# Performance work log

Measured on AMD Instinct MI355X. Metric: run time of the kernel, lower is better.

Reference implementation:

```python
import jax, jax.numpy as jnp
import numpy as np

N_SIGMA = 1
K_MAX = 8          # max number of non-zero instance ids
FG_W = 1.0         # foreground_weight
W_INST, W_VAR, W_SEED = 1.0, 10.0, 1.0


def _lovasz_hinge_flat(logits, labels_f):
    # logits, labels_f: [P] flat; standard Lovasz hinge (descending-error sort)
    signs = 2.0 * labels_f - 1.0
    errors = 1.0 - logits * signs
    perm = jnp.argsort(-errors)
    errors_sorted = errors[perm]
    gt_sorted = labels_f[perm]
    gts = gt_sorted.sum()
    cum = jnp.cumsum(gt_sorted)
    intersection = gts - cum
    union = gts + jnp.cumsum(1.0 - gt_sorted)
    jaccard = 1.0 - intersection / union
    grad = jnp.concatenate([jaccard[:1], jaccard[1:] - jaccard[:-1]])
    return jnp.sum(jax.nn.relu(errors_sorted) * jax.lax.stop_gradient(grad))


def _spatial_emb_loss(prediction, instances, labels):
    B, C, H, W = prediction.shape
    inst = instances[:, 0]  # [B,H,W]
    # coordinate buffer: linspace over the full 1024x2048 grid, then sliced
    xm = jnp.linspace(0.0, 2.0, 2048)[:W]
    ym = jnp.linspace(0.0, 1.0, 1024)[:H]
    xym = jnp.stack([jnp.broadcast_to(xm[None, :], (H, W)),
                     jnp.broadcast_to(ym[:, None], (H, W))])  # [2,H,W]
    ids = jnp.arange(1, K_MAX + 1)

    def per_image(pred, ins, lab):
        spatial_emb = jnp.tanh(pred[0:2]) + xym            # [2,H,W]
        sigma = pred[2]                                     # [H,W] (n_sigma=1)
        seed = jax.nn.sigmoid(pred[3])                      # [H,W]
        bg = (lab == 0)
        seed_loss_bg = jnp.sum(jnp.where(bg, seed ** 2, 0.0))
        masks = (ins[None] == ids[:, None, None])           # [K,H,W]
        mf = masks.astype(pred.dtype)
        counts = mf.sum((1, 2))                             # [K]
        present = counts > 0
        cnt = jnp.maximum(counts, 1.0)
        # to_center=True: center = mean of xym over instance pixels
        center = jnp.einsum('chw,khw->kc', xym, mf) / cnt[:, None]   # [K,2]
        s_mean = jnp.einsum('hw,khw->k', sigma, mf) / cnt            # [K]
        var_k = jnp.einsum('khw,khw->k',
                           (sigma[None] - jax.lax.stop_gradient(s_mean)[:, None, None]) ** 2,
                           mf) / cnt
        s_exp = jnp.exp(10.0 * s_mean)                                # [K]
        d2 = jnp.sum((spatial_emb[None] - center[:, :, None, None]) ** 2, axis=1)  # [K,H,W]
        dist = jnp.exp(-s_exp[:, None, None] * d2)                    # [K,H,W]
        lov = jax.vmap(_lovasz_hinge_flat)(2.0 * dist.reshape(K_MAX, -1) - 1.0,
                                           mf.reshape(K_MAX, -1))     # [K]
        seed_fg = jnp.einsum('khw,khw->k',
                             (seed[None] - jax.lax.stop_gradient(dist)) ** 2, mf)
        objf = jnp.maximum(present.sum().astype(pred.dtype), 1.0)
        inst_loss = jnp.where(present, lov, 0.0).sum() / objf
        var_loss = jnp.where(present, var_k, 0.0).sum() / objf
        seed_loss = (seed_loss_bg + FG_W * jnp.where(present, seed_fg, 0.0).sum()) / (H * W)
        return W_INST * inst_loss + W_VAR * var_loss + W_SEED * seed_loss

    per = jax.vmap(per_image)(prediction, inst, labels)
    return per.mean() + 0.0 * prediction.sum()


def setup_inputs() -> dict:
    key = jax.random.key(0)
    k1, k2, k3 = jax.random.split(key, 3)
    B, H, W = 4, 512, 1024
    prediction = jax.random.normal(k1, (B, 2 + N_SIGMA + 1, H, W), dtype=jnp.float32)
    instances = jax.random.randint(k2, (B, 1, H, W), 0, K_MAX + 1, dtype=jnp.int32)
    labels = jax.random.randint(k3, (B, H, W), 0, 2, dtype=jnp.int32)
    return {"prediction": prediction, "instances": instances, "labels": labels}


def reference(prediction, instances, labels):
    return _spatial_emb_loss(prediction, instances, labels)
```

## Files before the change

### kernel.cpp

```cpp
#include <hip/hip_runtime.h>
#include <math.h>

namespace {
constexpr int B_ = 4, K_ = 8, H_ = 512, W_ = 1024;
constexpr int N_ = H_ * W_;
constexpr int M_ = 256;
constexpr int MP_ = M_ + 1;
constexpr int BK_ = B_ * K_;
constexpr int KM_ = K_ * M_;

constexpr int HB_ = 2048;
constexpr int HBPB_ = HB_ / B_;
constexpr int HCH_ = N_ / HBPB_;
constexpr int SB_ = 1024;
constexpr int SBPB_ = SB_ / B_;
constexpr int SCH_ = N_ / SBPB_;
constexpr int NSTAT = 41;
constexpr int SLICES_ = 8;

constexpr size_t PART_BYTES  = (size_t)HB_ * KM_ * 4;
constexpr size_t SFG_OFF_B   = PART_BYTES;
constexpr size_t RED_OFF_B   = SFG_OFF_B + (size_t)BK_ * HBPB_ * 4;
constexpr size_t PSTAT_OFF_B = RED_OFF_B + (size_t)BK_ * SLICES_ * M_ * 8;
constexpr size_t WSF_OFF_B   = PSTAT_OFF_B + (size_t)B_ * NSTAT * SBPB_ * 4;

constexpr int CNT_OFF  = 0;
constexpr int BG_OFF   = 32;
constexpr int OBJF_OFF = 36;
constexpr int FIN_OFF  = 40;
}

__device__ __forceinline__ float fsigmoid_(float x) { return 1.0f / (1.0f + __expf(-x)); }
__device__ __forceinline__ float ftanh_(float x) { return 1.0f - 2.0f / (__expf(2.0f * x) + 1.0f); }

__global__ __launch_bounds__(256) void stats_kernel(const float* __restrict__ pred,
                                                    const int* __restrict__ inst,
                                                    const int* __restrict__ lab,
                                                    float* __restrict__ pstat) {
    int tid = threadIdx.x;
    int b = blockIdx.x >> 8;
    int blk = blockIdx.x & (SBPB_ - 1);
    int pix0 = blk * SCH_;

    const float* sigp = pred + ((long long)b * 4 + 2) * N_;
    const float* p3p  = pred + ((long long)b * 4 + 3) * N_;
    const int*   insp = inst + (long long)b * N_;
    const int*   labp = lab  + (long long)b * N_;

    float acc[NSTAT];
#pragma unroll
    for (int i = 0; i < NSTAT; i++) acc[i] = 0.0f;

#pragma unroll
    for (int it = 0; it < SCH_ / (256 * 4); it++) {
        int base = pix0 + (it * 256 + tid) * 4;
        float4 sg = *(const float4*)(sigp + base);
        float4 q3 = *(const float4*)(p3p + base);
        int4 in4 = *(const int4*)(insp + base);
        int4 lb4 = *(const int4*)(labp + base);
        float ss[4] = {sg.x, sg.y, sg.z, sg.w};
        float qq[4] = {q3.x, q3.y, q3.z, q3.w};
        int ii[4] = {in4.x, in4.y, in4.z, in4.w};
        int ll[4] = {lb4.x, lb4.y, lb4.z, lb4.w};
#pragma unroll
        for (int j = 0; j < 4; j++) {
            int pix = base + j;
            float xm = (float)(pix & (W_ - 1)) * (2.0f / 2047.0f);
            float ym = (float)(pix >> 10) * (1.0f / 1023.0f);
            float seed = fsigmoid_(qq[j]);
            if (ll[j] == 0) acc[40] += seed * seed;
            float s = ss[j];
#pragma unroll
            for (int k = 0; k < K_; k++) {
                float m = (ii[j] == k + 1) ? 1.0f : 0.0f;
                acc[k * 5]     += m;
                acc[k * 5 + 1] += m * xm;
                acc[k * 5 + 2] += m * ym;
                acc[k * 5 + 3] += m * s;
                acc[k * 5 + 4] += m * s * s;
            }
        }
    }
#pragma unroll
    for (int i = 0; i < NSTAT; i++) {
        float v = acc[i];
#pragma unroll
        for (int off = 32; off; off >>= 1) v += __shfl_down(v, off, 64);
        acc[i] = v;
    }
    __shared__ float xw[4][NSTAT];
    if ((tid & 63) == 0) {
        int w = tid >> 6;
#pragma unroll
        for (int i = 0; i < NSTAT; i++) xw[w][i] = acc[i];
    }
    __syncthreads();
    if (tid < NSTAT)
        pstat[((b * NSTAT + tid) << 8) + blk] =
            xw[0][tid] + xw[1][tid] + xw[2][tid] + xw[3][tid];
}

__global__ void finalize_kernel(const float* __restrict__ pstat, float* __restrict__ wsf,
                                float* __restrict__ out) {
    __shared__ float sums[B_][NSTAT];
    __shared__ float svar[BK_];
    __shared__ int spres[BK_];
    int t = threadIdx.x;
    if (t < B_ * NSTAT) {
        const float4* p = (const float4*)(pstat + ((size_t)t << 8));
        float4 a = {0, 0, 0, 0};
        for (int j = 0; j < SBPB_ / 4; j++) {
            float4 v = p[j];
            a.x += v.x; a.y += v.y; a.z += v.z; a.w += v.w;
        }
        sums[t / NSTAT][t % NSTAT] = (a.x + a.y) + (a.z + a.w);
    }
    __syncthreads();
    if (t < BK_) {
        int b = t >> 3, k = t & 7;
        float counts = sums[b][k * 5];
        float cnt = fmaxf(counts, 1.0f);
        float smean = sums[b][k * 5 + 3] / cnt;
        float var = sums[b][k * 5 + 4] / cnt - smean * smean;
        float* fin = wsf + FIN_OFF + t * 5;
        fin[0] = sums[b][k * 5 + 1] / cnt;
        fin[1] = sums[b][k * 5 + 2] / cnt;
        fin[2] = expf(10.0f * smean);
        fin[3] = counts;
        fin[4] = var;
        wsf[CNT_OFF + t] = counts;
        svar[t] = var;
        spres[t] = counts > 0.0f ? 1 : 0;
    }
    __syncthreads();
    if (t == 0) {
        float o = 0.0f;
        for (int b = 0; b < B_; b++) {
            float npres = 0.0f, varl = 0.0f;
            for (int k = 0; k < K_; k++) {
                if (spres[b * K_ + k]) { npres += 1.0f; varl += svar[b * K_ + k]; }
            }
            float objf = fmaxf(npres, 1.0f);
            wsf[OBJF_OFF + b] = objf;
            wsf[BG_OFF + b] = sums[b][40];
            o += 10.0f * varl / objf + sums[b][40] / (float)N_;
        }
        out[0] = o * (1.0f / (float)B_);
    }
}

__global__ __launch_bounds__(256) void hist_kernel(const float* __restrict__ pred,
                                                   const int* __restrict__ inst,
                                                   const float* __restrict__ wsf,
                                                   unsigned int* __restrict__ partial,
                                                   float* __restrict__ sfgpart) {
    __shared__ unsigned int hsh[K_ * MP_];
    __shared__ float xfg[4][K_];
    int tid = threadIdx.x;
    int b = blockIdx.x >> 9;
    int blk = blockIdx.x & (HBPB_ - 1);
    int pix0 = blk * HCH_;

    for (int i = tid; i < K_ * MP_; i += 256) hsh[i] = 0u;

    float cx[K_], cy[K_], sxp[K_];
    bool prs[K_];
#pragma unroll
    for (int k = 0; k < K_; k++) {
        const float* fin = wsf + FIN_OFF + (b * K_ + k) * 5;
        cx[k] = fin[0]; cy[k] = fin[1]; sxp[k] = fin[2];
        prs[k] = fin[3] > 0.0f;
    }
    __syncthreads();

    const float* p0p = pred + ((long long)b * 4) * N_;
    const float* p1p = p0p + N_;
    const float* p3p = p0p + 3LL * N_;
    const int* insp = inst + (long long)b * N_;

    float sfg[K_];
#pragma unroll
    for (int k = 0; k < K_; k++) sfg[k] = 0.0f;

    {
        int base = pix0 + tid * 4;
        float4 a0 = *(const float4*)(p0p + base);
        float4 a1 = *(const float4*)(p1p + base);
        float4 a3 = *(const float4*)(p3p + base);
        int4 in4 = *(const int4*)(insp + base);
        float v0[4] = {a0.x, a0.y, a0.z, a0.w};
        float v1[4] = {a1.x, a1.y, a1.z, a1.w};
        float v3[4] = {a3.x, a3.y, a3.z, a3.w};
        int ii[4] = {in4.x, in4.y, in4.z, in4.w};
#pragma unroll
        for (int j = 0; j < 4; j++) {
            int pix = base + j;
            float sex = ftanh_(v0[j]) + (float)(pix & (W_ - 1)) * (2.0f / 2047.0f);
            float sey = ftanh_(v1[j]) + (float)(pix >> 10) * (1.0f / 1023.0f);
            float seed = fsigmoid_(v3[j]);
            int ins = ii[j];
#pragma unroll
            for (int k = 0; k < K_; k++) {
                if (prs[k]) {
                    float dx = sex - cx[k];
                    float dy = sey - cy[k];
                    float dist = __expf(-sxp[k] * (dx * dx + dy * dy));
                    bool fg = (ins == k + 1);
                    int ib = (int)fminf(256.0f * dist, 255.0f);
                    int bin = fg ? 255 - ib : ib;
                    atomicAdd(&hsh[k * MP_ + bin], fg ? 0x10001u : 1u);
                    if (fg) { float d = seed - dist; sfg[k] += d * d; }
                }
            }
        }
    }
    __syncthreads();

    unsigned int* gp = partial + (size_t)blockIdx.x * KM_;
    for (int i = tid; i < KM_; i += 256)
        gp[i] = hsh[(i >> 8) * MP_ + (i & (M_ - 1))];

#pragma unroll
    for (int k = 0; k < K_; k++) {
        float v = sfg[k];
#pragma unroll
        for (int off = 32; off; off >>= 1) v += __shfl_down(v, off, 64);
        sfg[k] = v;
    }
    if ((tid & 63) == 0) {
        int w = tid >> 6;
#pragma unroll
        for (int k = 0; k < K_; k++) xfg[w][k] = sfg[k];
    }
    __syncthreads();
    if (tid < K_)
        sfgpart[(size_t)(b * K_ + tid) * HBPB_ + blk] =
            xfg[0][tid] + xfg[1][tid] + xfg[2][tid] + xfg[3][tid];
}

__global__ __launch_bounds__(256) void reduce_kernel(const unsigned int* __restrict__ partial,
                                                     uint2* __restrict__ red) {
    int bk = blockIdx.x >> 3;
    int s  = blockIdx.x & (SLICES_ - 1);
    int b = bk >> 3, k = bk & 7;
    int tid = threadIdx.x;
    constexpr int PER = HBPB_ / SLICES_;

    const unsigned int* p = partial + (size_t)(b * HBPB_ + s * PER) * KM_ + k * M_ + tid;
    unsigned int n = 0, f = 0;
#pragma unroll 8
    for (int j = 0; j < PER; j++) {
        unsigned int v = p[(size_t)j * KM_];
        n += v & 0xffffu;
        f += v >> 16;
    }
    red[(size_t)(bk * SLICES_ + s) * M_ + tid] = make_uint2(n, f);
}

__global__ __launch_bounds__(256) void lovasz_kernel(const uint2* __restrict__ red,
                                                     const float* __restrict__ sfgpart,
                                                     const float* __restrict__ wsf,
                                                     float* __restrict__ out) {
    int bk = blockIdx.x;
    int b = bk >> 3;
    int tid = threadIdx.x;

    unsigned int n = 0, f = 0;
#pragma unroll
    for (int s = 0; s < SLICES_; s++) {
        uint2 v = red[(size_t)(bk * SLICES_ + s) * M_ + tid];
        n += v.x; f += v.y;
    }

    __shared__ unsigned int sn[256], sf[256];
    __shared__ float sacc[256];
    __shared__ float xs[4];
    sn[tid] = n; sf[tid] = f;
    __syncthreads();
#pragma unroll
    for (int s = 1; s < 256; s <<= 1) {
        unsigned an = sn[tid], af = sf[tid];
        unsigned bn = 0, bf = 0;
        if (tid + s < 256) { bn = sn[tid + s]; bf = sf[tid + s]; }
        __syncthreads();
        sn[tid] = an + bn; sf[tid] = af + bf;
        __syncthreads();
    }

    float pcnt = wsf[CNT_OFF + bk];
    float pp = fmaxf(pcnt, 1.0f);
    unsigned int R = sn[tid], F = sf[tid];
    float J = (R == 0) ? 0.0f : (1.0f - (pp - (float)F) / (pp + (float)(R - F)));
    sacc[tid] = (tid == 0 ? 0.5f : 1.0f) * J;
    __syncthreads();
    for (int s = 128; s > 0; s >>= 1) {
        if (tid < s) sacc[tid] += sacc[tid + s];
        __syncthreads();
    }

    const float* sp = sfgpart + (size_t)bk * HBPB_;
    float sv = sp[tid] + sp[tid + 256];
#pragma unroll
    for (int off = 32; off; off >>= 1) sv += __shfl_down(sv, off, 64);
    if ((tid & 63) == 0) xs[tid >> 6] = sv;
    __syncthreads();

    if (tid == 0 && pcnt > 0.0f) {
        float lov = sacc[0] * (2.0f / (float)M_);
        float sfgt = (xs[0] + xs[1]) + (xs[2] + xs[3]);
        float objf = wsf[OBJF_OFF + b];
        atomicAdd(out, (lov / objf + sfgt / (float)N_) * (1.0f / (float)B_));
    }
}

extern "C" void kernel_launch(void* const* d_in, const int* in_sizes, int n_in,
                              void* d_out, int out_size, void* d_ws, size_t ws_size,
                              hipStream_t stream) {
    const float* pred = (const float*)d_in[0];
    const int* inst = (const int*)d_in[1];
    const int* lab = (const int*)d_in[2];
    float* out = (float*)d_out;

    unsigned int* partial = (unsigned int*)d_ws;
    float* sfgpart = (float*)((char*)d_ws + SFG_OFF_B);
    uint2* red = (uint2*)((char*)d_ws + RED_OFF_B);
    float* pstat = (float*)((char*)d_ws + PSTAT_OFF_B);
    float* wsf = (float*)((char*)d_ws + WSF_OFF_B);

    stats_kernel<<<SB_, 256, 0, stream>>>(pred, inst, lab, pstat);
    finalize_kernel<<<1, 256, 0, stream>>>(pstat, wsf, out);
    hist_kernel<<<HB_, 256, 0, stream>>>(pred, inst, wsf, partial, sfgpart);
    reduce_kernel<<<BK_ * SLICES_, 256, 0, stream>>>(partial, red);
    lovasz_kernel<<<BK_, 256, 0, stream>>>(red, sfgpart, wsf, out);
}
```

Before: 128.5 us.

## Fuse finalize into hist and reduce into lovasz, halve hist blocks

Removes the single-block finalize kernel by having each hist block re-reduce the per-image stats partials itself, with block 0 of each image writing the count, objf and variance/bg contribution. Hist blocks drop to 1024 and each processes two iterations, which halves the partial-histogram volume. The separate reduce kernel is folded into a 1024-thread lovasz kernel that sums the partials over four groups. This cuts launches from five to three and reduces workspace traffic, at the cost of redundant stats reductions per hist block and only 32 blocks doing the partial reduction.

```diff
diff --git a/kernel.cpp b/kernel.cpp
--- a/kernel.cpp
+++ b/kernel.cpp
@@ -9,25 +9,21 @@
 constexpr int BK_ = B_ * K_;
 constexpr int KM_ = K_ * M_;
 
-constexpr int HB_ = 2048;
+constexpr int HB_ = 1024;
 constexpr int HBPB_ = HB_ / B_;
 constexpr int HCH_ = N_ / HBPB_;
 constexpr int SB_ = 1024;
 constexpr int SBPB_ = SB_ / B_;
 constexpr int SCH_ = N_ / SBPB_;
 constexpr int NSTAT = 41;
-constexpr int SLICES_ = 8;
-
-constexpr size_t PART_BYTES  = (size_t)HB_ * KM_ * 4;
-constexpr size_t SFG_OFF_B   = PART_BYTES;
-constexpr size_t RED_OFF_B   = SFG_OFF_B + (size_t)BK_ * HBPB_ * 4;
-constexpr size_t PSTAT_OFF_B = RED_OFF_B + (size_t)BK_ * SLICES_ * M_ * 8;
-constexpr size_t WSF_OFF_B   = PSTAT_OFF_B + (size_t)B_ * NSTAT * SBPB_ * 4;
+
+constexpr size_t PART_BYTES = (size_t)HB_ * KM_ * 4;
+constexpr size_t SFG_OFF_B  = PART_BYTES;
+constexpr size_t PSTAT_OFF_B = SFG_OFF_B + (size_t)BK_ * HBPB_ * 4;
+constexpr size_t WSF_OFF_B  = PSTAT_OFF_B + (size_t)B_ * NSTAT * SBPB_ * 4;
 
 constexpr int CNT_OFF  = 0;
-constexpr int BG_OFF   = 32;
-constexpr int OBJF_OFF = 36;
-constexpr int FIN_OFF  = 40;
+constexpr int OBJF_OFF = 32;
 }
 
 __device__ __forceinline__ float fsigmoid_(float x) { return 1.0f / (1.0f + __expf(-x)); }
@@ -36,8 +32,10 @@
 __global__ __launch_bounds__(256) void stats_kernel(const float* __restrict__ pred,
                                                     const int* __restrict__ inst,
                                                     const int* __restrict__ lab,
-                                                    float* __restrict__ pstat) {
+                                                    float* __restrict__ pstat,
+                                                    float* __restrict__ out) {
     int tid = threadIdx.x;
+    if (blockIdx.x == 0 && tid == 0) out[0] = 0.0f;
     int b = blockIdx.x >> 8;
     int blk = blockIdx.x & (SBPB_ - 1);
     int pix0 = blk * SCH_;
@@ -100,78 +98,72 @@
             xw[0][tid] + xw[1][tid] + xw[2][tid] + xw[3][tid];
 }
 
-__global__ void finalize_kernel(const float* __restrict__ pstat, float* __restrict__ wsf,
-                                float* __restrict__ out) {
-    __shared__ float sums[B_][NSTAT];
-    __shared__ float svar[BK_];
-    __shared__ int spres[BK_];
-    int t = threadIdx.x;
-    if (t < B_ * NSTAT) {
-        const float4* p = (const float4*)(pstat + ((size_t)t << 8));
+__global__ __launch_bounds__(256) void hist_kernel(const float* __restrict__ pred,
+                                                   const int* __restrict__ inst,
+                                                   const float* __restrict__ pstat,
+                                                   float* __restrict__ wsf,
+                                                   unsigned int* __restrict__ partial,
+                                                   float* __restrict__ sfgpart,
+                                                   float* __restrict__ out) {
+    __shared__ float sq[NSTAT][4];
+    __shared__ float ssum[NSTAT];
+    __shared__ float prm[K_][4];
+    __shared__ float svar[K_];
+    __shared__ int spres[K_];
+    __shared__ unsigned int hsh[K_ * MP_];
+    __shared__ float xfg[4][K_];
+
+    int tid = threadIdx.x;
+    int b = blockIdx.x >> 8;
+    int blk = blockIdx.x & (HBPB_ - 1);
+    int pix0 = blk * HCH_;
+
+    if (tid < NSTAT * 4) {
+        int row = tid >> 2, q = tid & 3;
+        const float4* p = (const float4*)(pstat + ((size_t)(b * NSTAT + row) << 8)) + q * 16;
         float4 a = {0, 0, 0, 0};
-        for (int j = 0; j < SBPB_ / 4; j++) {
+#pragma unroll
+        for (int j = 0; j < 16; j++) {
             float4 v = p[j];
             a.x += v.x; a.y += v.y; a.z += v.z; a.w += v.w;
         }
-        sums[t / NSTAT][t % NSTAT] = (a.x + a.y) + (a.z + a.w);
-    }
-    __syncthreads();
-    if (t < BK_) {
-        int b = t >> 3, k = t & 7;
-        float counts = sums[b][k * 5];
+        sq[row][q] = (a.x + a.y) + (a.z + a.w);
+    }
+    for (int i = tid; i < K_ * MP_; i += 256) hsh[i] = 0u;
+    __syncthreads();
+    if (tid < NSTAT) ssum[tid] = (sq[tid][0] + sq[tid][1]) + (sq[tid][2] + sq[tid][3]);
+    __syncthreads();
+    if (tid < K_) {
+        float counts = ssum[tid * 5];
         float cnt = fmaxf(counts, 1.0f);
-        float smean = sums[b][k * 5 + 3] / cnt;
-        float var = sums[b][k * 5 + 4] / cnt - smean * smean;
-        float* fin = wsf + FIN_OFF + t * 5;
-        fin[0] = sums[b][k * 5 + 1] / cnt;
-        fin[1] = sums[b][k * 5 + 2] / cnt;
-        fin[2] = expf(10.0f * smean);
-        fin[3] = counts;
-        fin[4] = var;
-        wsf[CNT_OFF + t] = counts;
-        svar[t] = var;
-        spres[t] = counts > 0.0f ? 1 : 0;
-    }
-    __syncthreads();
-    if (t == 0) {
-        float o = 0.0f;
-        for (int b = 0; b < B_; b++) {
-            float npres = 0.0f, varl = 0.0f;
-            for (int k = 0; k < K_; k++) {
-                if (spres[b * K_ + k]) { npres += 1.0f; varl += svar[b * K_ + k]; }
-            }
-            float objf = fmaxf(npres, 1.0f);
-            wsf[OBJF_OFF + b] = objf;
-            wsf[BG_OFF + b] = sums[b][40];
-            o += 10.0f * varl / objf + sums[b][40] / (float)N_;
-        }
-        out[0] = o * (1.0f / (float)B_);
-    }
-}
-
-__global__ __launch_bounds__(256) void hist_kernel(const float* __restrict__ pred,
-                                                   const int* __restrict__ inst,
-                                                   const float* __restrict__ wsf,
-                                                   unsigned int* __restrict__ partial,
-                                                   float* __restrict__ sfgpart) {
-    __shared__ unsigned int hsh[K_ * MP_];
-    __shared__ float xfg[4][K_];
-    int tid = threadIdx.x;
-    int b = blockIdx.x >> 9;
-    int blk = blockIdx.x & (HBPB_ - 1);
-    int pix0 = blk * HCH_;
-
-    for (int i = tid; i < K_ * MP_; i += 256) hsh[i] = 0u;
+        float smean = ssum[tid * 5 + 3] / cnt;
+        prm[tid][0] = ssum[tid * 5 + 1] / cnt;
+        prm[tid][1] = ssum[tid * 5 + 2] / cnt;
+        prm[tid][2] = expf(10.0f * smean);
+        prm[tid][3] = counts;
+        if (blk == 0) {
+            svar[tid] = (counts > 0.0f) ? ssum[tid * 5 + 4] / cnt - smean * smean : 0.0f;
+            spres[tid] = counts > 0.0f ? 1 : 0;
+            wsf[CNT_OFF + b * K_ + tid] = counts;
+        }
+    }
+    __syncthreads();
+    if (blk == 0 && tid == 0) {
+        float np = 0.0f, vl = 0.0f;
+#pragma unroll
+        for (int k = 0; k < K_; k++) { np += (float)spres[k]; vl += svar[k]; }
+        float objf = fmaxf(np, 1.0f);
+        wsf[OBJF_OFF + b] = objf;
+        atomicAdd(out, (10.0f * vl / objf + ssum[40] / (float)N_) * (1.0f / (float)B_));
+    }
 
     float cx[K_], cy[K_], sxp[K_];
     bool prs[K_];
 #pragma unroll
     for (int k = 0; k < K_; k++) {
-        const float* fin = wsf + FIN_OFF + (b * K_ + k) * 5;
-        cx[k] = fin[0]; cy[k] = fin[1]; sxp[k] = fin[2];
-        prs[k] = fin[3] > 0.0f;
-    }
-    __syncthreads();
+        cx[k] = prm[k][0]; cy[k] = prm[k][1]; sxp[k] = prm[k][2];
+        prs[k] = prm[k][3] > 0.0f;
+    }
 
     const float* p0p = pred + ((long long)b * 4) * N_;
     const float* p1p = p0p + N_;
@@ -182,8 +174,9 @@
 #pragma unroll
     for (int k = 0; k < K_; k++) sfg[k] = 0.0f;
 
-    {
-        int base = pix0 + tid * 4;
+#pragma unroll
+    for (int it = 0; it < HCH_ / (256 * 4); it++) {
+        int base = pix0 + (it * 256 + tid) * 4;
         float4 a0 = *(const float4*)(p0p + base);
         float4 a1 = *(const float4*)(p1p + base);
         float4 a3 = *(const float4*)(p3p + base);
@@ -238,15 +231,18 @@
             xfg[0][tid] + xfg[1][tid] + xfg[2][tid] + xfg[3][tid];
 }
 
-__global__ __launch_bounds__(256) void reduce_kernel(const unsigned int* __restrict__ partial,
-                                                     uint2* __restrict__ red) {
-    int bk = blockIdx.x >> 3;
-    int s  = blockIdx.x & (SLICES_ - 1);
+__global__ __launch_bounds__(1024) void lovasz_kernel(const unsigned int* __restrict__ partial,
+                                                      const float* __restrict__ sfgpart,
+                                                      const float* __restrict__ wsf,
+                                                      float* __restrict__ out) {
+    int bk = blockIdx.x;
     int b = bk >> 3, k = bk & 7;
     int tid = threadIdx.x;
-    constexpr int PER = HBPB_ / SLICES_;
-
-    const unsigned int* p = partial + (size_t)(b * HBPB_ + s * PER) * KM_ + k * M_ + tid;
+    int bin = tid & 255, grp = tid >> 8;
+    constexpr int PER = HBPB_ / 4;
+
+    const unsigned int* p = partial +
+        (size_t)(b * HBPB_ + grp * PER) * KM_ + k * M_ + bin;
     unsigned int n = 0, f = 0;
 #pragma unroll 8
     for (int j = 0; j < PER; j++) {
@@ -254,55 +250,48 @@
         n += v & 0xffffu;
         f += v >> 16;
     }
-    red[(size_t)(bk * SLICES_ + s) * M_ + tid] = make_uint2(n, f);
-}
-
-__global__ __launch_bounds__(256) void lovasz_kernel(const uint2* __restrict__ red,
-                                                     const float* __restrict__ sfgpart,
-                                                     const float* __restrict__ wsf,
-                                                     float* __restrict__ out) {
-    int bk = blockIdx.x;
-    int b = bk >> 3;
-    int tid = threadIdx.x;
-
-    unsigned int n = 0, f = 0;
-#pragma unroll
-    for (int s = 0; s < SLICES_; s++) {
-        uint2 v = red[(size_t)(bk * SLICES_ + s) * M_ + tid];
-        n += v.x; f += v.y;
-    }
-
+
+    __shared__ unsigned int gn[4][256], gf[4][256];
     __shared__ unsigned int sn[256], sf[256];
     __shared__ float sacc[256];
     __shared__ float xs[4];
-    sn[tid] = n; sf[tid] = f;
-    __syncthreads();
+    gn[grp][bin] = n; gf[grp][bin] = f;
+    __syncthreads();
+    if (grp == 0) {
+        sn[bin] = (gn[0][bin] + gn[1][bin]) + (gn[2][bin] + gn[3][bin]);
+        sf[bin] = (gf[0][bin] + gf[1][bin]) + (gf[2][bin] + gf[3][bin]);
+    }
+    __syncthreads();
+
 #pragma unroll
     for (int s = 1; s < 256; s <<= 1) {
-        unsigned an = sn[tid], af = sf[tid];
-        unsigned bn = 0, bf = 0;
-        if (tid + s < 256) { bn = sn[tid + s]; bf = sf[tid + s]; }
+        unsigned int an = 0, af = 0, bn = 0, bf = 0;
+        if (tid < 256) {
+            an = sn[tid]; af = sf[tid];
+            if (tid + s < 256) { bn = sn[tid + s]; bf = sf[tid + s]; }
+        }
         __syncthreads();
-        sn[tid] = an + bn; sf[tid] = af + bf;
+        if (tid < 256) { sn[tid] = an + bn; sf[tid] = af + bf; }
         __syncthreads();
     }
 
     float pcnt = wsf[CNT_OFF + bk];
     float pp = fmaxf(pcnt, 1.0f);
-    unsigned int R = sn[tid], F = sf[tid];
-    float J = (R == 0) ? 0.0f : (1.0f - (pp - (float)F) / (pp + (float)(R - F)));
-    sacc[tid] = (tid == 0 ? 0.5f : 1.0f) * J;
+    if (tid < 256) {
+        unsigned int R = sn[tid], F = sf[tid];
+        float J = (R == 0) ? 0.0f : (1.0f - (pp - (float)F) / (pp + (float)(R - F)));
+        sacc[tid] = (tid == 0 ? 0.5f : 1.0f) * J;
+    }
     __syncthreads();
     for (int s = 128; s > 0; s >>= 1) {
         if (tid < s) sacc[tid] += sacc[tid + s];
         __syncthreads();
     }
 
-    const float* sp = sfgpart + (size_t)bk * HBPB_;
-    float sv = sp[tid] + sp[tid + 256];
+    float sv = (tid < 256) ? sfgpart[(size_t)bk * HBPB_ + tid] : 0.0f;
 #pragma unroll
     for (int off = 32; off; off >>= 1) sv += __shfl_down(sv, off, 64);
-    if ((tid & 63) == 0) xs[tid >> 6] = sv;
+    if (tid < 256 && (tid & 63) == 0) xs[tid >> 6] = sv;
     __syncthreads();
 
     if (tid == 0 && pcnt > 0.0f) {
@@ -323,13 +312,10 @@
 
     unsigned int* partial = (unsigned int*)d_ws;
     float* sfgpart = (float*)((char*)d_ws + SFG_OFF_B);
-    uint2* red = (uint2*)((char*)d_ws + RED_OFF_B);
     float* pstat = (float*)((char*)d_ws + PSTAT_OFF_B);
     float* wsf = (float*)((char*)d_ws + WSF_OFF_B);
 
-    stats_kernel<<<SB_, 256, 0, stream>>>(pred, inst, lab, pstat);
-    finalize_kernel<<<1, 256, 0, stream>>>(pstat, wsf, out);
-    hist_kernel<<<HB_, 256, 0, stream>>>(pred, inst, wsf, partial, sfgpart);
-    reduce_kernel<<<BK_ * SLICES_, 256, 0, stream>>>(partial, red);
-    lovasz_kernel<<<BK_, 256, 0, stream>>>(red, sfgpart, wsf, out);
-}
+    stats_kernel<<<SB_, 256, 0, stream>>>(pred, inst, lab, pstat, out);
+    hist_kernel<<<HB_, 256, 0, stream>>>(pred, inst, pstat, wsf, partial, sfgpart, out);
+    lovasz_kernel<<<BK_, 1024, 0, stream>>>(partial, sfgpart, wsf, out);
+}
```

Result: faster. 121.1 us (-5.8%).
